# Kernel optimization log

Measured on AMD Instinct MI355X. Metric: run time of the kernel, lower is better.

The kernel has to match this reference:

```python
import jax, jax.numpy as jnp
import numpy as np
from jax import lax

DN = ('NCHW', 'OIHW', 'NCHW')

def conv(x, w, b, stride=1):
    y = lax.conv_general_dilated(x, w, window_strides=(stride, stride),
                                 padding='VALID', dimension_numbers=DN)
    return y + b[None, :, None, None]

def maxpool(x, k=3, s=2):
    return lax.reduce_window(x, -jnp.inf, lax.max,
                             (1, 1, k, k), (1, 1, s, s), 'VALID')

def setup_inputs() -> dict:
    key = jax.random.key(0)
    ks = jax.random.split(key, 7)
    B = 2048
    x = jax.random.normal(ks[0], (B, 1, 28, 28), dtype=jnp.float32)
    w1 = jax.random.normal(ks[1], (64, 1, 3, 3), dtype=jnp.float32)
    b1 = jax.random.normal(ks[2], (64,), dtype=jnp.float32)
    w2 = jax.random.normal(ks[3], (64, 64, 3, 3), dtype=jnp.float32)
    b2 = jax.random.normal(ks[4], (64,), dtype=jnp.float32)
    w3 = jax.random.normal(ks[5], (10, 64, 4, 4), dtype=jnp.float32)
    b3 = jax.random.normal(ks[6], (10,), dtype=jnp.float32)
    return {"x": x, "w1": w1, "b1": b1, "w2": w2, "b2": b2, "w3": w3, "b3": b3}

def reference(x, w1, b1, w2, b2, w3, b3):
    h = conv(x, w1, b1)            # [B,64,26,26]
    h = maxpool(h)                 # [B,64,12,12]
    h = jnp.maximum(h, 0.0)
    h = conv(h, w2, b2)            # [B,64,10,10]
    h = maxpool(h)                 # [B,64,4,4]
    h = jnp.maximum(h, 0.0)
    h = conv(h, w3, b3)            # [B,10,1,1]
    return h.reshape(h.shape[0], -1)  # [B,10]
```

## Files before the change

kernel.cpp:

```cpp
#include <hip/hip_runtime.h>


typedef __attribute__((ext_vector_type(8))) short short8;
typedef __attribute__((ext_vector_type(4))) float f32x4;

__device__ inline short f2bf(float f) {
    union { float f; unsigned u; } v; v.f = f;
    unsigned r = (v.u + 0x7FFFu + ((v.u >> 16) & 1u)) >> 16;
    return (short)r;
}

__global__ __launch_bounds__(256) void prep_w2(const float* __restrict__ w2,
                                               short* __restrict__ w2r) {
    int i = blockIdx.x * 256 + threadIdx.x;
    if (i >= 36864) return;
    int s = i >> 12, cout = (i >> 6) & 63, cin = i & 63;
    w2r[i] = f2bf(w2[cout * 576 + cin * 9 + s]);
}

__global__ __launch_bounds__(256) void convnet_fused(
    const float* __restrict__ x,
    const float* __restrict__ w1,
    const float* __restrict__ b1,
    const short* __restrict__ w2r,
    const float* __restrict__ b2,
    const float* __restrict__ w3,
    const float* __restrict__ b3,
    float* __restrict__ out)
{
    __shared__ float lds_f[7488];
    short* h1t  = (short*)lds_f;
    float* img  = lds_f + 5184;
    float* cbuf = lds_f;
    float* h2t  = lds_f + 6464;
    float* prt  = lds_f;

    const int n_img = blockIdx.x;
    const int t = threadIdx.x;
    const int c = t >> 2;
    const int q = t & 3;

    const float* img_g = x + (size_t)n_img * 784;
    for (int i = t; i < 784; i += 256) img[i] = img_g[i];
    __syncthreads();

    {
        const int oy = (q >> 1) * 6, ox = (q & 1) * 6;
        const int iy0 = 2 * oy, ix0 = 2 * ox;
        float w[9];
        #pragma unroll
        for (int k = 0; k < 9; ++k) w[k] = w1[c * 9 + k];
        const float bias = b1[c];

        float rows[3][16];
        {
            const float* s0 = img + iy0 * 28 + ix0;
            const float* s1 = img + (iy0 + 1) * 28 + ix0;
            #pragma unroll
            for (int m = 0; m < 4; ++m) {
                *(float4*)(rows[0] + 4 * m) = *(const float4*)(s0 + 4 * m);
                *(float4*)(rows[1] + 4 * m) = *(const float4*)(s1 + 4 * m);
            }
        }
        float cm[3][6];

        #pragma unroll
        for (int r = 0; r < 13; ++r) {
            {
                const float* s2 = img + (iy0 + r + 2) * 28 + ix0;
                float* dst = rows[(r + 2) % 3];
                #pragma unroll
                for (int m = 0; m < 4; ++m)
                    *(float4*)(dst + 4 * m) = *(const float4*)(s2 + 4 * m);
            }
            const float* r0 = rows[r % 3];
            const float* r1 = rows[(r + 1) % 3];
            const float* r2 = rows[(r + 2) % 3];
            #pragma unroll
            for (int px = 0; px < 6; ++px) cm[r % 3][px] = -1e30f;
            #pragma unroll
            for (int xx = 0; xx < 13; ++xx) {
                float a = bias;
                #pragma unroll
                for (int j = 0; j < 3; ++j) {
                    a += r0[xx + j] * w[j];
                    a += r1[xx + j] * w[3 + j];
                    a += r2[xx + j] * w[6 + j];
                }
                if ((xx & 1) == 0) {
                    if (xx >= 2 && xx <= 12) cm[r % 3][xx / 2 - 1] = fmaxf(cm[r % 3][xx / 2 - 1], a);
                    if (xx <= 10)            cm[r % 3][xx / 2]     = fmaxf(cm[r % 3][xx / 2], a);
                } else {
                    cm[r % 3][xx / 2] = fmaxf(cm[r % 3][xx / 2], a);
                }
            }
            if (r >= 2 && (r & 1) == 0) {
                const int py = r / 2 - 1;
                #pragma unroll
                for (int px = 0; px < 6; ++px) {
                    float m = fmaxf(fmaxf(cm[0][px], cm[1][px]), cm[2][px]);
                    h1t[((oy + py) * 12 + ox + px) * 72 + c] = f2bf(fmaxf(m, 0.0f));
                }
            }
        }
    }
    __syncthreads();

    const int wv = t >> 6, lane = t & 63;
    const int quad = lane >> 4, mrow = lane & 15;
    {
        int base_el[7];
        #pragma unroll
        for (int nt = 0; nt < 7; ++nt) {
            int n = nt * 16 + mrow; if (n > 99) n = 99;
            int y = n / 10, xx = n - y * 10;
            base_el[nt] = (y * 12 + xx) * 72;
        }
        f32x4 acc[7];
        #pragma unroll
        for (int nt = 0; nt < 7; ++nt) acc[nt] = (f32x4){0.f, 0.f, 0.f, 0.f};

        #pragma unroll
        for (int ks = 0; ks < 18; ++ks) {
            const int s = ks >> 1, h = ks & 1;
            const int ky = s / 3, kx = s - ky * 3;
            const short8 a = *(const short8*)(w2r + s * 4096 + (wv * 16 + mrow) * 64
                                              + h * 32 + quad * 8);
            #pragma unroll
            for (int nt = 0; nt < 7; ++nt) {
                const short8 b = *(const short8*)(h1t + base_el[nt]
                                                  + (ky * 12 + kx) * 72 + h * 32 + quad * 8);
                acc[nt] = __builtin_amdgcn_mfma_f32_16x16x32_bf16(a, b, acc[nt], 0, 0, 0);
            }
        }
        __syncthreads();
        #pragma unroll
        for (int nt = 0; nt < 7; ++nt) {
            const int n = nt * 16 + mrow;
            if (n < 100) {
                #pragma unroll
                for (int r = 0; r < 4; ++r) {
                    const int co = wv * 16 + quad * 4 + r;
                    cbuf[co * 101 + n] = acc[nt][r] + b2[co];
                }
            }
        }
    }
    __syncthreads();

    {
        const float* cb = cbuf + c * 101;
        #pragma unroll
        for (int k = 0; k < 4; ++k) {
            const int pos = q * 4 + k;
            const int py = pos >> 2, px = pos & 3;
            float m = -1e30f;
            #pragma unroll
            for (int a = 0; a < 3; ++a)
                #pragma unroll
                for (int b = 0; b < 3; ++b)
                    m = fmaxf(m, cb[(2 * py + a) * 10 + (2 * px + b)]);
            h2t[pos * 64 + c] = fmaxf(m, 0.0f);
        }
    }
    __syncthreads();

    if (t < 160) {
        const int o = t >> 4, g = t & 15;
        const float* w3o = w3 + o * 1024 + g * 64;
        float wr[4][16];
        #pragma unroll
        for (int cc = 0; cc < 4; ++cc)
            #pragma unroll
            for (int m = 0; m < 4; ++m)
                *(float4*)(wr[cc] + 4 * m) = *(const float4*)(w3o + cc * 16 + 4 * m);
        float s = 0.0f;
        #pragma unroll
        for (int pos = 0; pos < 16; ++pos) {
            const float4 hv = *(const float4*)(h2t + pos * 64 + g * 4);
            s += hv.x * wr[0][pos] + hv.y * wr[1][pos] + hv.z * wr[2][pos] + hv.w * wr[3][pos];
        }
        prt[t] = s;
    }
    __syncthreads();
    if (t < 10) {
        float s = b3[t];
        #pragma unroll
        for (int g = 0; g < 16; ++g) s += prt[t * 16 + g];
        out[(size_t)n_img * 10 + t] = s;
    }
}

extern "C" void kernel_launch(void* const* d_in, const int* in_sizes, int n_in,
                              void* d_out, int out_size, void* d_ws, size_t ws_size,
                              hipStream_t stream) {
    const float* x  = (const float*)d_in[0];
    const float* w1 = (const float*)d_in[1];
    const float* b1 = (const float*)d_in[2];
    const float* w2 = (const float*)d_in[3];
    const float* b2 = (const float*)d_in[4];
    const float* w3 = (const float*)d_in[5];
    const float* b3 = (const float*)d_in[6];
    float* out = (float*)d_out;
    short* w2r = (short*)d_ws;

    const int B = in_sizes[0] / 784;
    prep_w2<<<144, 256, 0, stream>>>(w2, w2r);
    convnet_fused<<<B, 256, 0, stream>>>(x, w1, b1, w2r, b2, w3, b3, out);
}
```

Measured before the change: 112.0 us.

## Repartition conv2 MFMA tiling across waves and simplify conv1 pooling

Conv2 work is repartitioned: each wave now covers all 64 output channels over two 16-pixel N tiles (8 tiles total, 128 >= 100 positions), instead of 16 channels over seven N tiles. This cuts the redundant padded tiles from 112 to 128 columns split evenly and changes A/B reuse, trading more weight loads per wave for fewer LDS activation loads. The image load is vectorized to float4. Conv1 column pooling is rewritten to compute a row of 13 values and then take the maxima, removing the branchy per-element updates.

```diff
diff --git a/kernel.cpp b/kernel.cpp
--- a/kernel.cpp
+++ b/kernel.cpp
@@ -40,8 +40,11 @@
     const int c = t >> 2;
     const int q = t & 3;
 
-    const float* img_g = x + (size_t)n_img * 784;
-    for (int i = t; i < 784; i += 256) img[i] = img_g[i];
+    {
+        const float4* src4 = (const float4*)(x + (size_t)n_img * 784);
+        float4* dst4 = (float4*)img;
+        if (t < 196) dst4[t] = src4[t];
+    }
     __syncthreads();
 
     {
@@ -76,24 +79,21 @@
             const float* r0 = rows[r % 3];
             const float* r1 = rows[(r + 1) % 3];
             const float* r2 = rows[(r + 2) % 3];
-            #pragma unroll
-            for (int px = 0; px < 6; ++px) cm[r % 3][px] = -1e30f;
+            float a[13];
             #pragma unroll
             for (int xx = 0; xx < 13; ++xx) {
-                float a = bias;
+                float v = bias;
                 #pragma unroll
                 for (int j = 0; j < 3; ++j) {
-                    a += r0[xx + j] * w[j];
-                    a += r1[xx + j] * w[3 + j];
-                    a += r2[xx + j] * w[6 + j];
+                    v += r0[xx + j] * w[j];
+                    v += r1[xx + j] * w[3 + j];
+                    v += r2[xx + j] * w[6 + j];
                 }
-                if ((xx & 1) == 0) {
-                    if (xx >= 2 && xx <= 12) cm[r % 3][xx / 2 - 1] = fmaxf(cm[r % 3][xx / 2 - 1], a);
-                    if (xx <= 10)            cm[r % 3][xx / 2]     = fmaxf(cm[r % 3][xx / 2], a);
-                } else {
-                    cm[r % 3][xx / 2] = fmaxf(cm[r % 3][xx / 2], a);
-                }
-            }
+                a[xx] = v;
+            }
+            #pragma unroll
+            for (int px = 0; px < 6; ++px)
+                cm[r % 3][px] = fmaxf(fmaxf(a[2 * px], a[2 * px + 1]), a[2 * px + 2]);
             if (r >= 2 && (r & 1) == 0) {
                 const int py = r / 2 - 1;
                 #pragma unroll
@@ -109,40 +109,50 @@
     const int wv = t >> 6, lane = t & 63;
     const int quad = lane >> 4, mrow = lane & 15;
     {
-        int base_el[7];
-        #pragma unroll
-        for (int nt = 0; nt < 7; ++nt) {
-            int n = nt * 16 + mrow; if (n > 99) n = 99;
+        int base_el[2];
+        #pragma unroll
+        for (int nt = 0; nt < 2; ++nt) {
+            int n = (wv * 2 + nt) * 16 + mrow;
+            if (n > 99) n = 99;
             int y = n / 10, xx = n - y * 10;
             base_el[nt] = (y * 12 + xx) * 72;
         }
-        f32x4 acc[7];
-        #pragma unroll
-        for (int nt = 0; nt < 7; ++nt) acc[nt] = (f32x4){0.f, 0.f, 0.f, 0.f};
+        f32x4 acc[4][2];
+        #pragma unroll
+        for (int mt = 0; mt < 4; ++mt)
+            #pragma unroll
+            for (int nt = 0; nt < 2; ++nt) acc[mt][nt] = (f32x4){0.f, 0.f, 0.f, 0.f};
 
         #pragma unroll
         for (int ks = 0; ks < 18; ++ks) {
             const int s = ks >> 1, h = ks & 1;
             const int ky = s / 3, kx = s - ky * 3;
-            const short8 a = *(const short8*)(w2r + s * 4096 + (wv * 16 + mrow) * 64
-                                              + h * 32 + quad * 8);
-            #pragma unroll
-            for (int nt = 0; nt < 7; ++nt) {
-                const short8 b = *(const short8*)(h1t + base_el[nt]
-                                                  + (ky * 12 + kx) * 72 + h * 32 + quad * 8);
-                acc[nt] = __builtin_amdgcn_mfma_f32_16x16x32_bf16(a, b, acc[nt], 0, 0, 0);
+            const int cinb = h * 32 + quad * 8;
+            short8 a[4];
+            #pragma unroll
+            for (int mt = 0; mt < 4; ++mt)
+                a[mt] = *(const short8*)(w2r + s * 4096 + (mt * 16 + mrow) * 64 + cinb);
+            const int toff = (ky * 12 + kx) * 72 + cinb;
+            #pragma unroll
+            for (int nt = 0; nt < 2; ++nt) {
+                const short8 b = *(const short8*)(h1t + base_el[nt] + toff);
+                #pragma unroll
+                for (int mt = 0; mt < 4; ++mt)
+                    acc[mt][nt] = __builtin_amdgcn_mfma_f32_16x16x32_bf16(a[mt], b, acc[mt][nt], 0, 0, 0);
             }
         }
         __syncthreads();
         #pragma unroll
-        for (int nt = 0; nt < 7; ++nt) {
-            const int n = nt * 16 + mrow;
+        for (int nt = 0; nt < 2; ++nt) {
+            const int n = (wv * 2 + nt) * 16 + mrow;
             if (n < 100) {
                 #pragma unroll
-                for (int r = 0; r < 4; ++r) {
-                    const int co = wv * 16 + quad * 4 + r;
-                    cbuf[co * 101 + n] = acc[nt][r] + b2[co];
-                }
+                for (int mt = 0; mt < 4; ++mt)
+                    #pragma unroll
+                    for (int r = 0; r < 4; ++r) {
+                        const int co = mt * 16 + quad * 4 + r;
+                        cbuf[co * 101 + n] = acc[mt][nt][r] + b2[co];
+                    }
             }
         }
     }
```

Result: slower. 154.6 us (+38.0%).
